# Kernel optimization log

Measured on AMD Instinct MI355X. Metric: run time of the kernel, lower is better.

The kernel has to match this reference:

```python
import jax, jax.numpy as jnp
import numpy as np

B, N, C = 2, 2048, 1536
H = 8
D = C // H  # 192, must match M's size


def setup_inputs() -> dict:
    key = jax.random.key(0)
    ks = jax.random.split(key, 5)
    x = jax.random.normal(ks[0], (B, N, C), dtype=jnp.float32)
    # nn.Linear(dim, 3*dim, bias=False): weight shape (3C, C)
    W_qkv = jax.random.normal(ks[1], (3 * C, C), dtype=jnp.float32) * (C ** -0.5)
    # nn.Linear(dim, dim) with bias
    W_proj = jax.random.normal(ks[2], (C, C), dtype=jnp.float32) * (C ** -0.5)
    b_proj = jnp.zeros((C,), dtype=jnp.float32)
    scale = jnp.asarray(D ** -0.5, dtype=jnp.float32)  # learned scalar, init head_dim**-0.5
    M = jnp.eye(D, dtype=jnp.float32)  # learned Mahalanobis metric, init identity
    return {"x": x, "W_qkv": W_qkv, "W_proj": W_proj, "b_proj": b_proj,
            "scale": scale, "M": M}


def reference(x, W_qkv, W_proj, b_proj, scale, M):
    Bv, Nv, Cv = x.shape
    qkv = x @ W_qkv.T                                  # [B,N,3C]
    qkv = qkv.reshape(Bv, Nv, 3, H, D).transpose(2, 0, 3, 1, 4)  # [3,B,H,N,D]
    q, k, v = qkv[0], qkv[1], qkv[2]
    q_M = q @ M                                        # [B,H,N,D]
    k_M = k @ M                                        # [B,H,N,D]
    qMq = jnp.sum(q * q_M, axis=-1, keepdims=True)     # [B,H,N,1]
    kMk = jnp.sum(k * k_M, axis=-1, keepdims=True)     # [B,H,N,1]
    kMk = jnp.swapaxes(kMk, -2, -1)                    # [B,H,1,N]
    qMk = jnp.einsum('bhnd,bhmd->bhnm', q_M, k)        # [B,H,N,N]
    dists = qMq + kMk - 2.0 * qMk                      # Mahalanobis quadratic form
    attn = jax.nn.softmax(-dists * scale, axis=-1)     # [B,H,N,N]
    out = jnp.einsum('bhnm,bhmd->bhnd', attn, v)       # [B,H,N,D]
    out = jnp.swapaxes(out, 1, 2).reshape(Bv, Nv, Cv)  # [B,N,C]
    out = out @ W_proj.T + b_proj
    return (out, attn, M)
```

## Files before the change

### kernel.cpp

```cpp
#include <hip/hip_runtime.h>

typedef _Float16 f16;
typedef __attribute__((ext_vector_type(8))) _Float16 f16x8;
typedef __attribute__((ext_vector_type(4))) float f32x4;

#define LOG2E 1.4426950408889634f
#define MFMA16(a, b, c) __builtin_amdgcn_mfma_f32_16x16x32_f16((a), (b), (c), 0, 0, 0)


__device__ __forceinline__ void gl16(const void* g, void* l) {
    __builtin_amdgcn_global_load_lds(
        (const __attribute__((address_space(1))) unsigned int*)g,
        (__attribute__((address_space(3))) unsigned int*)l, 16, 0, 0);
}

__global__ void k_cvt_all(const float* __restrict__ x, const float* __restrict__ wq,
                          const float* __restrict__ wp, f16* __restrict__ xh,
                          f16* __restrict__ wqh, f16* __restrict__ wph) {
    int i = blockIdx.x * 256 + threadIdx.x;
    const float4* s; short4* d; int off;
    if (i < 1572864) { s = (const float4*)x; d = (short4*)xh; off = i; }
    else if (i < 3342336) { s = (const float4*)wq; d = (short4*)wqh; off = i - 1572864; }
    else { s = (const float4*)wp; d = (short4*)wph; off = i - 3342336; }
    float4 v = s[off];
    union { f16 h[4]; short4 s4; } u;
    u.h[0] = (f16)v.x; u.h[1] = (f16)v.y; u.h[2] = (f16)v.z; u.h[3] = (f16)v.w;
    d[off] = u.s4;
}

__global__ void k_cvtM(const float* __restrict__ M, f16* __restrict__ Mt) {
    int i = blockIdx.x * 256 + threadIdx.x;
    if (i >= 192 * 192) return;
    int d = i / 192, e = i - (i / 192) * 192;
    Mt[d * 192 + e] = (f16)M[e * 192 + d];
}

__global__ __launch_bounds__(256) void k_gemm_qkv(
    const f16* __restrict__ A, const f16* __restrict__ Bw,
    f16* __restrict__ Qh, f16* __restrict__ Kh, f16* __restrict__ Vp)
{
    __shared__ __align__(16) char S[32768];
    const int tid = threadIdx.x, lane = tid & 63, w = tid >> 6;
    const int bid = blockIdx.x;
    const int xcd = bid & 7, cc = bid >> 3;
    const int mb = xcd * 4 + cc / 36, nb = cc - (cc / 36) * 36;
    const int m0 = mb * 128, n0 = nb * 128;
    const int sec = nb >= 24 ? 2 : (nb >= 12 ? 1 : 0);
    const int wm = (w & 1) * 64, wn = (w >> 1) * 64;
    const int L = lane & 15, g = lane >> 4;
    const char* Ab = (const char*)A;
    const char* Bb = (const char*)Bw;

    const char* gA[2]; const char* gB[2]; int ldso[2];
#pragma unroll
    for (int q = 0; q < 2; ++q) {
        int s = w * 128 + q * 64 + lane;
        int swz = ((s & 3) ^ ((s >> 2) & 3)) * 16;
        gA[q] = Ab + (size_t)(m0 + (s >> 2)) * 3072 + swz;
        gB[q] = Bb + (size_t)(n0 + (s >> 2)) * 3072 + swz;
        ldso[q] = w * 2048 + q * 1024;
    }
    const int gx = ((g ^ (L & 3)) << 4);

    f32x4 acc[4][4] = {};
#pragma unroll
    for (int q = 0; q < 2; ++q) {
        gl16(gA[q], S + ldso[q]);
        gl16(gB[q], S + 8192 + ldso[q]);
    }
    int buf = 0;
    for (int kk = 0; kk < 48; ++kk) {
        __syncthreads();
        if (kk < 47) {
            int nb_ = (buf ^ 1) * 16384;
#pragma unroll
            for (int q = 0; q < 2; ++q) {
                gl16(gA[q] + (kk + 1) * 64, S + nb_ + ldso[q]);
                gl16(gB[q] + (kk + 1) * 64, S + nb_ + 8192 + ldso[q]);
            }
        }
        const char* AsB = S + buf * 16384;
        const char* BsB = AsB + 8192;
        f16x8 af[4], bf[4];
#pragma unroll
        for (int i = 0; i < 4; ++i) {
            af[i] = *(const f16x8*)(AsB + (wm + i * 16 + L) * 64 + gx);
            bf[i] = *(const f16x8*)(BsB + (wn + i * 16 + L) * 64 + gx);
        }
        if (sec < 2) {
#pragma unroll
            for (int i = 0; i < 4; ++i)
#pragma unroll
                for (int j = 0; j < 4; ++j)
                    acc[i][j] = MFMA16(bf[j], af[i], acc[i][j]);
        } else {
#pragma unroll
            for (int i = 0; i < 4; ++i)
#pragma unroll
                for (int j = 0; j < 4; ++j)
                    acc[i][j] = MFMA16(af[i], bf[j], acc[i][j]);
        }
        buf ^= 1;
    }

    if (sec == 2) {
#pragma unroll
        for (int i = 0; i < 4; ++i)
#pragma unroll
            for (int j = 0; j < 4; ++j) {
                int rem = n0 + wn + j * 16 + L - 3072;
                int h = rem / 192, d = rem - h * 192;
                int gm = m0 + wm + i * 16 + g * 4;
                int gb = gm >> 11, nn = gm & 2047;
                union { f16 h4[4]; short4 s4; } u;
#pragma unroll
                for (int r = 0; r < 4; ++r) u.h4[r] = (f16)acc[i][j][r];
                int nnp = (nn & ~31) | (((nn >> 2) & 3) << 3) | (((nn >> 4) & 1) << 2) | (nn & 3);
                *(short4*)(Vp + (size_t)((gb * 8 + h) * 192 + d) * 2048 + nnp) = u.s4;
            }
    } else {
        f16* base = sec == 0 ? Qh : Kh;
#pragma unroll
        for (int i = 0; i < 4; ++i) {
            int gm = m0 + wm + i * 16 + L;
            int gb = gm >> 11, nn = gm & 2047;
#pragma unroll
            for (int j = 0; j < 4; ++j) {
                int rem = n0 + wn + j * 16 + g * 4 - sec * 1536;
                int h = rem / 192, d = rem - h * 192;
                union { f16 h4[4]; short4 s4; } u;
#pragma unroll
                for (int r = 0; r < 4; ++r) u.h4[r] = (f16)acc[i][j][r];
                *(short4*)(base + (size_t)((gb * 8 + h) * 2048 + nn) * 192 + d) = u.s4;
            }
        }
    }
}

__global__ __launch_bounds__(256) void k_mgemm(
    const f16* __restrict__ Qh, const f16* __restrict__ Kh,
    const f16* __restrict__ Mt, f16* __restrict__ QMh,
    const float* __restrict__ scale_p, float* __restrict__ qmq, float* __restrict__ kmk)
{
    const int tid = threadIdx.x, lane = tid & 63, w = tid >> 6;
    const int L = lane & 15, g = lane >> 4;
    const int isK = blockIdx.y;
    const f16* src = isK ? Kh : Qh;
    float* rowdot = isK ? kmk : qmq;
    const int row0 = blockIdx.x * 64 + w * 16;
    const int tokrow = row0 + L;
    f16x8 af[6];
#pragma unroll
    for (int ks = 0; ks < 6; ++ks)
        af[ks] = *(const f16x8*)((const char*)src + (size_t)tokrow * 384 + ks * 64 + g * 16);
    f32x4 acc[12] = {};
#pragma unroll
    for (int ct = 0; ct < 12; ++ct)
#pragma unroll
        for (int ks = 0; ks < 6; ++ks) {
            f16x8 bf = *(const f16x8*)((const char*)Mt + (ct * 16 + L) * 384 + ks * 64 + g * 16);
            acc[ct] = MFMA16(bf, af[ks], acc[ct]);
        }
    if (!isK) {
#pragma unroll
        for (int ct = 0; ct < 12; ++ct) {
            union { f16 h4[4]; short4 s4; } u;
#pragma unroll
            for (int r = 0; r < 4; ++r) u.h4[r] = (f16)acc[ct][r];
            *(short4*)(QMh + (size_t)tokrow * 192 + ct * 16 + g * 4) = u.s4;
        }
    }
    float s = 0.f;
#pragma unroll
    for (int ct = 0; ct < 12; ++ct) {
        union { short4 s4; f16 h[4]; } kv;
        kv.s4 = *(const short4*)(src + (size_t)tokrow * 192 + ct * 16 + g * 4);
#pragma unroll
        for (int r = 0; r < 4; ++r) s += acc[ct][r] * (float)kv.h[r];
    }
    s += __shfl_xor(s, 16); s += __shfl_xor(s, 32);
    if (lane < 16) rowdot[row0 + lane] = s * scale_p[0] * LOG2E;
}

__global__ __launch_bounds__(256) void k_stats(
    const f16* __restrict__ QMh, const f16* __restrict__ Kh,
    const float* __restrict__ kmk, const float* __restrict__ qmq,
    const float* __restrict__ scale_p, float* __restrict__ lhalf)
{
    __shared__ __align__(16) char KsB[2][12288];
    const int tid = threadIdx.x, lane = tid & 63, w = tid >> 6;
    const int L = lane & 15, g = lane >> 4;
    const int bx = blockIdx.x;
    const int xcd = bx & 7, cc = bx >> 3;
    const int bh = xcd * 2 + (cc >> 6);
    const int qb = (cc >> 1) & 31;
    const int kh = cc & 1;
    const int c0 = kh * 32;
    const int row0 = qb * 64 + w * 16;
    const float a2 = 2.f * scale_p[0] * LOG2E;

    const char* qbase = (const char*)QMh + (size_t)(bh * 2048 + row0) * 384;
    f16x8 qf[6];
#pragma unroll
    for (int ks = 0; ks < 6; ++ks)
        qf[ks] = *(const f16x8*)(qbase + L * 384 + ks * 64 + g * 16);
    const char* Kb = (const char*)Kh + (size_t)bh * 2048 * 384;
    const float* kmkrow = kmk + bh * 2048;
    const float Crow = qmq[bh * 2048 + row0 + L];

    int ksrc[3], kdst[3];
#pragma unroll
    for (int i = 0; i < 3; ++i) {
        int s = tid + 256 * i;
        int r = s / 24, c16 = s - r * 24;
        ksrc[i] = r * 384 + c16 * 16;
        kdst[i] = r * 384 + (((c16 & ~7) | ((c16 & 7) ^ (r & 7))) << 4);
    }
    int kslot[6];
#pragma unroll
    for (int ks = 0; ks < 6; ++ks) {
        int slot = ks * 4 + g;
        kslot[ks] = (((slot & ~7) | ((slot & 7) ^ (L & 7))) << 4);
    }
    int4 stk[3];
#pragma unroll
    for (int i = 0; i < 3; ++i) stk[i] = *(const int4*)(Kb + (size_t)c0 * 12288 + ksrc[i]);

    float lacc = 0.f;
    for (int cl = 0; cl < 32; ++cl) {
        const int c = c0 + cl;
        char* Kl = KsB[cl & 1];
#pragma unroll
        for (int i = 0; i < 3; ++i) *(int4*)(Kl + kdst[i]) = stk[i];
        if (cl < 31) {
#pragma unroll
            for (int i = 0; i < 3; ++i)
                stk[i] = *(const int4*)(Kb + (size_t)(c + 1) * 12288 + ksrc[i]);
        }
        __syncthreads();
        f32x4 a0 = {}, a1 = {};
#pragma unroll
        for (int ks = 0; ks < 6; ++ks) {
            f16x8 kf0 = *(const f16x8*)(Kl + L * 384 + kslot[ks]);
            f16x8 kf1 = *(const f16x8*)(Kl + (16 + L) * 384 + kslot[ks]);
            a0 = MFMA16(kf0, qf[ks], a0);
            a1 = MFMA16(kf1, qf[ks], a1);
        }
        float4 km0 = *(const float4*)(kmkrow + c * 32 + g * 4);
        float4 km1 = *(const float4*)(kmkrow + c * 32 + 16 + g * 4);
        lacc += __builtin_amdgcn_exp2f(a2 * a0[0] - km0.x - Crow);
        lacc += __builtin_amdgcn_exp2f(a2 * a0[1] - km0.y - Crow);
        lacc += __builtin_amdgcn_exp2f(a2 * a0[2] - km0.z - Crow);
        lacc += __builtin_amdgcn_exp2f(a2 * a0[3] - km0.w - Crow);
        lacc += __builtin_amdgcn_exp2f(a2 * a1[0] - km1.x - Crow);
        lacc += __builtin_amdgcn_exp2f(a2 * a1[1] - km1.y - Crow);
        lacc += __builtin_amdgcn_exp2f(a2 * a1[2] - km1.z - Crow);
        lacc += __builtin_amdgcn_exp2f(a2 * a1[3] - km1.w - Crow);
    }
    lacc += __shfl_xor(lacc, 16);
    lacc += __shfl_xor(lacc, 32);
    if (g == 0) lhalf[kh * 32768 + bh * 2048 + row0 + L] = lacc;
}

__global__ __launch_bounds__(256) void k_attn(
    const f16* __restrict__ QMh, const f16* __restrict__ Kh,
    const f16* __restrict__ Vp, const float* __restrict__ kmk,
    const float* __restrict__ qmq, const float* __restrict__ scale_p,
    const float* __restrict__ lhalf,
    float* __restrict__ attn, f16* __restrict__ ctx)
{
    __shared__ __align__(16) char KsB[2][12288];
    __shared__ __align__(16) char VsB[2][15360];
    const int tid = threadIdx.x, lane = tid & 63, w = tid >> 6;
    const int L = lane & 15, g = lane >> 4;
    const int bx = blockIdx.x;
    const int bh = (bx & 7) * 2 + (bx >> 8);
    const int qb = (bx >> 3) & 31;
    const int row0 = qb * 64 + w * 16;
    const float a2 = 2.f * scale_p[0] * LOG2E;

    const char* qbase = (const char*)QMh + (size_t)(bh * 2048 + row0) * 384;
    f16x8 qf[6];
#pragma unroll
    for (int ks = 0; ks < 6; ++ks)
        qf[ks] = *(const f16x8*)(qbase + L * 384 + ks * 64 + g * 16);
    const char* Kb = (const char*)Kh + (size_t)bh * 2048 * 384;
    const char* Vb = (const char*)Vp + (size_t)bh * 192 * 4096;
    const float* kmkrow = kmk + bh * 2048;
    const int rowi = bh * 2048 + row0 + L;
    const float moff = qmq[rowi] + __log2f(lhalf[rowi] + lhalf[32768 + rowi]);

    int ksrc[3], kdst[3], vsrc[3], vdst[3];
#pragma unroll
    for (int i = 0; i < 3; ++i) {
        int s = tid + 256 * i;
        int r = s / 24, c16 = s - r * 24;
        ksrc[i] = r * 384 + c16 * 16;
        kdst[i] = r * 384 + (((c16 & ~7) | ((c16 & 7) ^ (r & 7))) << 4);
        vsrc[i] = (s >> 2) * 4096 + (s & 3) * 16;
        vdst[i] = (s >> 2) * 80 + (s & 3) * 16;
    }
    int kslot[6];
#pragma unroll
    for (int ks = 0; ks < 6; ++ks) {
        int slot = ks * 4 + g;
        kslot[ks] = (((slot & ~7) | ((slot & 7) ^ (L & 7))) << 4);
    }

    int4 stk[3], stv[3];
#pragma unroll
    for (int i = 0; i < 3; ++i) {
        stk[i] = *(const int4*)(Kb + ksrc[i]);
        stv[i] = *(const int4*)(Vb + vsrc[i]);
    }
    f32x4 cacc[12] = {};
    float* arow = attn + (size_t)rowi * 2048;

    for (int c = 0; c < 64; ++c) {
        char* Kl = KsB[c & 1];
        char* Vl = VsB[c & 1];
#pragma unroll
        for (int i = 0; i < 3; ++i) {
            *(int4*)(Kl + kdst[i]) = stk[i];
            *(int4*)(Vl + vdst[i]) = stv[i];
        }
        if (c < 63) {
#pragma unroll
            for (int i = 0; i < 3; ++i) {
                stk[i] = *(const int4*)(Kb + (size_t)(c + 1) * 12288 + ksrc[i]);
                stv[i] = *(const int4*)(Vb + (size_t)(c + 1) * 64 + vsrc[i]);
            }
        }
        __syncthreads();
        f32x4 a0 = {}, a1 = {};
#pragma unroll
        for (int ks = 0; ks < 6; ++ks) {
            f16x8 kf0 = *(const f16x8*)(Kl + L * 384 + kslot[ks]);
            f16x8 kf1 = *(const f16x8*)(Kl + (16 + L) * 384 + kslot[ks]);
            a0 = MFMA16(kf0, qf[ks], a0);
            a1 = MFMA16(kf1, qf[ks], a1);
        }
        float4 km0 = *(const float4*)(kmkrow + c * 32 + g * 4);
        float4 km1 = *(const float4*)(kmkrow + c * 32 + 16 + g * 4);
        float p[8];
        p[0] = __builtin_amdgcn_exp2f(a2 * a0[0] - km0.x - moff);
        p[1] = __builtin_amdgcn_exp2f(a2 * a0[1] - km0.y - moff);
        p[2] = __builtin_amdgcn_exp2f(a2 * a0[2] - km0.z - moff);
        p[3] = __builtin_amdgcn_exp2f(a2 * a0[3] - km0.w - moff);
        p[4] = __builtin_amdgcn_exp2f(a2 * a1[0] - km1.x - moff);
        p[5] = __builtin_amdgcn_exp2f(a2 * a1[1] - km1.y - moff);
        p[6] = __builtin_amdgcn_exp2f(a2 * a1[2] - km1.z - moff);
        p[7] = __builtin_amdgcn_exp2f(a2 * a1[3] - km1.w - moff);
        *(float4*)(arow + c * 32 + g * 4)      = make_float4(p[0], p[1], p[2], p[3]);
        *(float4*)(arow + c * 32 + 16 + g * 4) = make_float4(p[4], p[5], p[6], p[7]);
        f16x8 pa;
        pa[0] = (f16)p[0]; pa[1] = (f16)p[1]; pa[2] = (f16)p[2]; pa[3] = (f16)p[3];
        pa[4] = (f16)p[4]; pa[5] = (f16)p[5]; pa[6] = (f16)p[6]; pa[7] = (f16)p[7];
#pragma unroll
        for (int dt = 0; dt < 12; ++dt) {
            f16x8 vf = *(const f16x8*)(Vl + (dt * 16 + L) * 80 + g * 16);
            cacc[dt] = MFMA16(pa, vf, cacc[dt]);
        }
    }

    __syncthreads();
    char* scr = (char*)KsB + w * 6144;
#pragma unroll
    for (int dt = 0; dt < 12; ++dt)
#pragma unroll
        for (int r = 0; r < 4; ++r)
            *(f16*)(scr + (g * 4 + r) * 384 + (dt * 16 + L) * 2) = (f16)cacc[dt][r];
    const int b = bh >> 3, h = bh & 7;
#pragma unroll
    for (int t = 0; t < 6; ++t) {
        int chunk = t * 64 + lane;
        int tok = chunk / 24, c16 = chunk - tok * 24;
        int4 v = *(const int4*)(scr + tok * 384 + c16 * 16);
        *(int4*)((char*)ctx + ((size_t)(b * 2048 + row0 + tok) * 1536 + h * 192) * 2 + c16 * 16) = v;
    }
}

__global__ __launch_bounds__(256) void k_proj(
    const f16* __restrict__ A, const f16* __restrict__ Bw,
    const float* __restrict__ bias, float* __restrict__ out)
{
    __shared__ __align__(16) char S[32768];
    const int tid = threadIdx.x, lane = tid & 63, w = tid >> 6;
    const int bid = blockIdx.x;
    const int xcd = bid & 7, cc = bid >> 3;
    const int mb = xcd * 4 + cc / 12, nbk = cc - (cc / 12) * 12;
    const int m0 = mb * 128, n0 = nbk * 128;
    const int wm = (w & 1) * 64, wn = (w >> 1) * 64;
    const int L = lane & 15, g = lane >> 4;
    const char* Ab = (const char*)A;
    const char* Bb = (const char*)Bw;

    const char* gA[2]; const char* gB[2]; int ldso[2];
#pragma unroll
    for (int q = 0; q < 2; ++q) {
        int s = w * 128 + q * 64 + lane;
        int swz = ((s & 3) ^ ((s >> 2) & 3)) * 16;
        gA[q] = Ab + (size_t)(m0 + (s >> 2)) * 3072 + swz;
        gB[q] = Bb + (size_t)(n0 + (s >> 2)) * 3072 + swz;
        ldso[q] = w * 2048 + q * 1024;
    }
    const int gx = ((g ^ (L & 3)) << 4);

    f32x4 acc[4][4] = {};
#pragma unroll
    for (int q = 0; q < 2; ++q) {
        gl16(gA[q], S + ldso[q]);
        gl16(gB[q], S + 8192 + ldso[q]);
    }
    int buf = 0;
    for (int kk = 0; kk < 48; ++kk) {
        __syncthreads();
        if (kk < 47) {
            int nb_ = (buf ^ 1) * 16384;
#pragma unroll
            for (int q = 0; q < 2; ++q) {
                gl16(gA[q] + (kk + 1) * 64, S + nb_ + ldso[q]);
                gl16(gB[q] + (kk + 1) * 64, S + nb_ + 8192 + ldso[q]);
            }
        }
        const char* AsB = S + buf * 16384;
        const char* BsB = AsB + 8192;
        f16x8 af[4], bf[4];
#pragma unroll
        for (int i = 0; i < 4; ++i) {
            af[i] = *(const f16x8*)(AsB + (wm + i * 16 + L) * 64 + gx);
            bf[i] = *(const f16x8*)(BsB + (wn + i * 16 + L) * 64 + gx);
        }
#pragma unroll
        for (int i = 0; i < 4; ++i)
#pragma unroll
            for (int j = 0; j < 4; ++j)
                acc[i][j] = MFMA16(bf[j], af[i], acc[i][j]);
        buf ^= 1;
    }
#pragma unroll
    for (int i = 0; i < 4; ++i) {
        int token = m0 + wm + i * 16 + L;
#pragma unroll
        for (int j = 0; j < 4; ++j) {
            int gnb = n0 + wn + j * 16 + g * 4;
            float4 bv = *(const float4*)(bias + gnb);
            float4 v = make_float4(acc[i][j][0] + bv.x, acc[i][j][1] + bv.y,
                                   acc[i][j][2] + bv.z, acc[i][j][3] + bv.w);
            *(float4*)(out + (size_t)token * 1536 + gnb) = v;
        }
    }
}

extern "C" void kernel_launch(void* const* d_in, const int* in_sizes, int n_in,
                              void* d_out, int out_size, void* d_ws, size_t ws_size,
                              hipStream_t stream)
{
    const float* x     = (const float*)d_in[0];
    const float* Wqkv  = (const float*)d_in[1];
    const float* Wproj = (const float*)d_in[2];
    const float* bproj = (const float*)d_in[3];
    const float* scale = (const float*)d_in[4];
    const float* M     = (const float*)d_in[5];
    float* out  = (float*)d_out;
    float* attn = out + 6291456;

    char* p = (char*)d_ws;
    f16* x_h     = (f16*)p;  p += 12582912;
    f16* Wqkv_h  = (f16*)p;  p += 14155776;
    f16* Wproj_h = (f16*)p;  p += 4718592;
    f16* Mt_h    = (f16*)p;  p += 73728;
    f16* Qh      = (f16*)p;  p += 12582912;
    f16* Kh      = (f16*)p;  p += 12582912;
    f16* Vp      = (f16*)p;  p += 12582912;
    f16* QMh     = (f16*)p;  p += 12582912;
    float* qmq   = (float*)p; p += 131072;
    float* kmk   = (float*)p; p += 131072;
    float* lhalf = (float*)p; p += 262144;
    f16* ctx     = (f16*)p;  p += 12582912;

    k_cvt_all<<<15360, 256, 0, stream>>>(x, Wqkv, Wproj, x_h, Wqkv_h, Wproj_h);
    k_cvtM<<<144, 256, 0, stream>>>(M, Mt_h);
    k_gemm_qkv<<<1152, 256, 0, stream>>>(x_h, Wqkv_h, Qh, Kh, Vp);
    k_mgemm<<<dim3(512, 2), 256, 0, stream>>>(Qh, Kh, Mt_h, QMh, scale, qmq, kmk);
    k_stats<<<1024, 256, 0, stream>>>(QMh, Kh, kmk, qmq, scale, lhalf);
    k_attn<<<512, 256, 0, stream>>>(QMh, Kh, Vp, kmk, qmq, scale, lhalf, attn, ctx);
    k_proj<<<384, 256, 0, stream>>>(ctx, Wproj_h, bproj, out);
    hipMemcpyAsync(out + 73400320, M, 36864 * 4, hipMemcpyDeviceToDevice, stream);
}
```

Measured before the change: 480.1 us.

## Split attention over key halves with fp32 partials and a combine kernel

The attention kernel now splits the key range into two halves, doubling the grid to 1024 blocks so more CUs stay busy. Each block writes fp32 partial context to a new workspace buffer, and a new k_comb kernel sums the two halves and converts to fp16 ctx. V is now single-buffered in LDS at the cost of an extra __syncthreads per iteration. The trade-off is about 50 MB of extra partial-sum traffic and one more kernel launch.

```diff
diff --git a/kernel.cpp b/kernel.cpp
--- a/kernel.cpp
+++ b/kernel.cpp
@@ -267,15 +267,18 @@
     const f16* __restrict__ Vp, const float* __restrict__ kmk,
     const float* __restrict__ qmq, const float* __restrict__ scale_p,
     const float* __restrict__ lhalf,
-    float* __restrict__ attn, f16* __restrict__ ctx)
+    float* __restrict__ attn, float* __restrict__ pacc)
 {
     __shared__ __align__(16) char KsB[2][12288];
-    __shared__ __align__(16) char VsB[2][15360];
+    __shared__ __align__(16) char VsB[15360];
     const int tid = threadIdx.x, lane = tid & 63, w = tid >> 6;
     const int L = lane & 15, g = lane >> 4;
     const int bx = blockIdx.x;
-    const int bh = (bx & 7) * 2 + (bx >> 8);
-    const int qb = (bx >> 3) & 31;
+    const int xcd = bx & 7, cc = bx >> 3;
+    const int bh = xcd * 2 + (cc >> 6);
+    const int qb = (cc >> 1) & 31;
+    const int kh = cc & 1;
+    const int c0 = kh * 32;
     const int row0 = qb * 64 + w * 16;
     const float a2 = 2.f * scale_p[0] * LOG2E;
 
@@ -310,28 +313,28 @@
     int4 stk[3], stv[3];
 #pragma unroll
     for (int i = 0; i < 3; ++i) {
-        stk[i] = *(const int4*)(Kb + ksrc[i]);
-        stv[i] = *(const int4*)(Vb + vsrc[i]);
+        stk[i] = *(const int4*)(Kb + (size_t)c0 * 12288 + ksrc[i]);
+        stv[i] = *(const int4*)(Vb + (size_t)c0 * 64 + vsrc[i]);
     }
     f32x4 cacc[12] = {};
     float* arow = attn + (size_t)rowi * 2048;
 
-    for (int c = 0; c < 64; ++c) {
-        char* Kl = KsB[c & 1];
-        char* Vl = VsB[c & 1];
-#pragma unroll
-        for (int i = 0; i < 3; ++i) {
-            *(int4*)(Kl + kdst[i]) = stk[i];
-            *(int4*)(Vl + vdst[i]) = stv[i];
-        }
-        if (c < 63) {
+    for (int cl = 0; cl < 32; ++cl) {
+        const int c = c0 + cl;
+        char* Kl = KsB[cl & 1];
+#pragma unroll
+        for (int i = 0; i < 3; ++i) *(int4*)(Kl + kdst[i]) = stk[i];
+        __syncthreads();
+#pragma unroll
+        for (int i = 0; i < 3; ++i) *(int4*)(VsB + vdst[i]) = stv[i];
+        __syncthreads();
+        if (cl < 31) {
 #pragma unroll
             for (int i = 0; i < 3; ++i) {
                 stk[i] = *(const int4*)(Kb + (size_t)(c + 1) * 12288 + ksrc[i]);
                 stv[i] = *(const int4*)(Vb + (size_t)(c + 1) * 64 + vsrc[i]);
             }
         }
-        __syncthreads();
         f32x4 a0 = {}, a1 = {};
 #pragma unroll
         for (int ks = 0; ks < 6; ++ks) {
@@ -358,26 +361,35 @@
         pa[4] = (f16)p[4]; pa[5] = (f16)p[5]; pa[6] = (f16)p[6]; pa[7] = (f16)p[7];
 #pragma unroll
         for (int dt = 0; dt < 12; ++dt) {
-            f16x8 vf = *(const f16x8*)(Vl + (dt * 16 + L) * 80 + g * 16);
+            f16x8 vf = *(const f16x8*)(VsB + (dt * 16 + L) * 80 + g * 16);
             cacc[dt] = MFMA16(pa, vf, cacc[dt]);
         }
     }
-
-    __syncthreads();
-    char* scr = (char*)KsB + w * 6144;
 #pragma unroll
     for (int dt = 0; dt < 12; ++dt)
 #pragma unroll
         for (int r = 0; r < 4; ++r)
-            *(f16*)(scr + (g * 4 + r) * 384 + (dt * 16 + L) * 2) = (f16)cacc[dt][r];
-    const int b = bh >> 3, h = bh & 7;
-#pragma unroll
-    for (int t = 0; t < 6; ++t) {
-        int chunk = t * 64 + lane;
-        int tok = chunk / 24, c16 = chunk - tok * 24;
-        int4 v = *(const int4*)(scr + tok * 384 + c16 * 16);
-        *(int4*)((char*)ctx + ((size_t)(b * 2048 + row0 + tok) * 1536 + h * 192) * 2 + c16 * 16) = v;
-    }
+            pacc[((size_t)kh * 32768 + bh * 2048 + row0 + g * 4 + r) * 192 + dt * 16 + L]
+                = cacc[dt][r];
+}
+
+__global__ __launch_bounds__(256) void k_comb(const float* __restrict__ pacc,
+                                              f16* __restrict__ ctx)
+{
+    int idx = blockIdx.x * 256 + threadIdx.x;
+    int row = idx / 24;
+    int d = (idx - row * 24) * 8;
+    const float* p0 = pacc + (size_t)row * 192 + d;
+    const float* p1 = p0 + (size_t)32768 * 192;
+    float4 a0 = *(const float4*)p0, a1 = *(const float4*)(p0 + 4);
+    float4 b0 = *(const float4*)p1, b1 = *(const float4*)(p1 + 4);
+    union { f16 h[8]; int4 v; } u;
+    u.h[0] = (f16)(a0.x + b0.x); u.h[1] = (f16)(a0.y + b0.y);
+    u.h[2] = (f16)(a0.z + b0.z); u.h[3] = (f16)(a0.w + b0.w);
+    u.h[4] = (f16)(a1.x + b1.x); u.h[5] = (f16)(a1.y + b1.y);
+    u.h[6] = (f16)(a1.z + b1.z); u.h[7] = (f16)(a1.w + b1.w);
+    int bh = row >> 11, nr = row & 2047;
+    *(int4*)(ctx + (size_t)((bh >> 3) * 2048 + nr) * 1536 + (bh & 7) * 192 + d) = u.v;
 }
 
 __global__ __launch_bounds__(256) void k_proj(
@@ -477,6 +489,7 @@
     float* qmq   = (float*)p; p += 131072;
     float* kmk   = (float*)p; p += 131072;
     float* lhalf = (float*)p; p += 262144;
+    float* pacc  = (float*)p; p += 50331648;
     f16* ctx     = (f16*)p;  p += 12582912;
 
     k_cvt_all<<<15360, 256, 0, stream>>>(x, Wqkv, Wproj, x_h, Wqkv_h, Wproj_h);
@@ -484,7 +497,8 @@
     k_gemm_qkv<<<1152, 256, 0, stream>>>(x_h, Wqkv_h, Qh, Kh, Vp);
     k_mgemm<<<dim3(512, 2), 256, 0, stream>>>(Qh, Kh, Mt_h, QMh, scale, qmq, kmk);
     k_stats<<<1024, 256, 0, stream>>>(QMh, Kh, kmk, qmq, scale, lhalf);
-    k_attn<<<512, 256, 0, stream>>>(QMh, Kh, Vp, kmk, qmq, scale, lhalf, attn, ctx);
+    k_attn<<<1024, 256, 0, stream>>>(QMh, Kh, Vp, kmk, qmq, scale, lhalf, attn, pacc);
+    k_comb<<<3072, 256, 0, stream>>>(pacc, ctx);
     k_proj<<<384, 256, 0, stream>>>(ctx, Wproj_h, bproj, out);
     hipMemcpyAsync(out + 73400320, M, 36864 * 4, hipMemcpyDeviceToDevice, stream);
 }
```

New measurement: 679.6 us. 41.6% more time.
